# Kernel optimization log

Hardware: AMD Instinct MI355X
Metric: run time of the kernel (lower is better)

The kernel has to match this reference:

```python
import jax, jax.numpy as jnp
import numpy as np

BATCH = 262144
LATENT_DIM = 128
N_CLUSTERS = 10


def setup_inputs() -> dict:
    key = jax.random.key(0)
    kz, kc = jax.random.split(key)
    z = jax.random.normal(kz, (BATCH, LATENT_DIM), dtype=jnp.float32)
    cluster_centers = jax.random.normal(kc, (N_CLUSTERS, LATENT_DIM), dtype=jnp.float32)
    return {"z": z, "cluster_centers": cluster_centers}


def reference(z, cluster_centers):
    # Student's-t soft assignment (alpha = 1):
    # q_ij = (1 + ||z_i - mu_j||^2)^-1, power ((alpha+1)/2) == 1
    # squared distances: [B, K]
    sq_dist = jnp.sum(jnp.square(z[:, None, :] - cluster_centers[None, :, :]), axis=2)
    q = 1.0 / (1.0 + sq_dist)
    q = q ** ((1.0 + 1.0) / 2.0)
    q = q / jnp.sum(q, axis=1, keepdims=True)  # row-normalize

    # target distribution p
    weight = q ** 2 / jnp.sum(q, axis=0)            # [B, K] / [K]
    p = weight / jnp.sum(weight, axis=1, keepdims=True)
    return (q, p)
```

## Files before the change

kernel.cpp:

```cpp
#include <hip/hip_runtime.h>
#include <stdint.h>

#define NB 262144
#define D 128
#define K 10

#define QBLOCKS 1024
#define QTHREADS 256
#define ROWS_PER_BLOCK (NB / QBLOCKS)
#define TILES_PER_WAVE (ROWS_PER_BLOCK / 4 / 16)

typedef __attribute__((ext_vector_type(8))) __bf16 bf16x8;
typedef __attribute__((ext_vector_type(4))) float f32x4;

__device__ inline __bf16 f2bf(float x) {
  unsigned u = __builtin_bit_cast(unsigned, x);
  u += 0x7fffu + ((u >> 16) & 1u);
  unsigned short s = (unsigned short)(u >> 16);
  return __builtin_bit_cast(__bf16, s);
}

__device__ inline bf16x8 make_frag(float4 lo, float4 hi) {
  bf16x8 a;
  a[0] = f2bf(lo.x); a[1] = f2bf(lo.y); a[2] = f2bf(lo.z); a[3] = f2bf(lo.w);
  a[4] = f2bf(hi.x); a[5] = f2bf(hi.y); a[6] = f2bf(hi.z); a[7] = f2bf(hi.w);
  return a;
}

__global__ __launch_bounds__(QTHREADS) void qkern(
    const float* __restrict__ z, const float* __restrict__ centers,
    float* __restrict__ qout, float* __restrict__ f) {
  __shared__ float red[4][16];

  const int t = threadIdx.x;
  const int w = t >> 6;
  const int lane = t & 63;
  const int n = lane & 15;
  const int g = lane >> 4;

  bf16x8 bfrag[4];
  float mu2 = 0.f;
  if (n < K) {
    const float* cp = centers + n * D;
#pragma unroll
    for (int c = 0; c < 4; ++c) {
      float4 lo = *reinterpret_cast<const float4*>(cp + c * 32 + g * 8);
      float4 hi = *reinterpret_cast<const float4*>(cp + c * 32 + g * 8 + 4);
      bfrag[c] = make_frag(lo, hi);
    }
#pragma unroll
    for (int d4 = 0; d4 < 32; ++d4) {
      float4 v = *reinterpret_cast<const float4*>(cp + d4 * 4);
      mu2 = fmaf(v.x, v.x, mu2); mu2 = fmaf(v.y, v.y, mu2);
      mu2 = fmaf(v.z, v.z, mu2); mu2 = fmaf(v.w, v.w, mu2);
    }
  } else {
    unsigned short zb = 0;
#pragma unroll
    for (int c = 0; c < 4; ++c)
#pragma unroll
      for (int j = 0; j < 8; ++j) bfrag[c][j] = __builtin_bit_cast(__bf16, zb);
  }

  float colp = 0.f;
  const int wbase = blockIdx.x * ROWS_PER_BLOCK + w * (TILES_PER_WAVE * 16);

  for (int tile = 0; tile < TILES_PER_WAVE; ++tile) {
    const int rbase = wbase + tile * 16;
    const float* zr = z + (size_t)(rbase + n) * D + g * 8;

    float4 zf[8];
#pragma unroll
    for (int c = 0; c < 4; ++c) {
      zf[2 * c]     = *reinterpret_cast<const float4*>(zr + c * 32);
      zf[2 * c + 1] = *reinterpret_cast<const float4*>(zr + c * 32 + 4);
    }

    float z2 = 0.f;
#pragma unroll
    for (int q8 = 0; q8 < 8; ++q8) {
      z2 = fmaf(zf[q8].x, zf[q8].x, z2); z2 = fmaf(zf[q8].y, zf[q8].y, z2);
      z2 = fmaf(zf[q8].z, zf[q8].z, z2); z2 = fmaf(zf[q8].w, zf[q8].w, z2);
    }
    z2 += __shfl_xor(z2, 16);
    z2 += __shfl_xor(z2, 32);

    f32x4 acc = {0.f, 0.f, 0.f, 0.f};
#pragma unroll
    for (int c = 0; c < 4; ++c) {
      bf16x8 a = make_frag(zf[2 * c], zf[2 * c + 1]);
      acc = __builtin_amdgcn_mfma_f32_16x16x32_bf16(a, bfrag[c], acc, 0, 0, 0);
    }

#pragma unroll
    for (int i = 0; i < 4; ++i) {
      float z2i = __shfl(z2, g * 4 + i);
      float d2 = z2i - 2.f * acc[i] + mu2;
      float qu = (n < K) ? 1.0f / (1.0f + d2) : 0.f;
      float rs = qu;
      rs += __shfl_xor(rs, 1); rs += __shfl_xor(rs, 2);
      rs += __shfl_xor(rs, 4); rs += __shfl_xor(rs, 8);
      float qv = qu * (1.0f / rs);
      if (n < K) qout[(size_t)(rbase + g * 4 + i) * K + n] = qv;
      colp += qv;
    }
  }

  colp += __shfl_xor(colp, 16);
  colp += __shfl_xor(colp, 32);
  if (lane < 16) red[w][lane] = colp;
  __syncthreads();
  if (t < K) atomicAdd(&f[t], red[0][t] + red[1][t] + red[2][t] + red[3][t]);
}

__global__ __launch_bounds__(256) void pkern(
    const float* __restrict__ q, const float* __restrict__ f,
    float* __restrict__ p) {
  int row = blockIdx.x * 256 + threadIdx.x;
  const float* qr = q + (size_t)row * K;
  float wv[K];
  float s = 0.f;
#pragma unroll
  for (int j = 0; j < K; j += 2) {
    float2 qq = *reinterpret_cast<const float2*>(&qr[j]);
    wv[j] = qq.x * qq.x / f[j];
    wv[j + 1] = qq.y * qq.y / f[j + 1];
    s += wv[j] + wv[j + 1];
  }
  float inv = 1.0f / s;
  float* pr = p + (size_t)row * K;
#pragma unroll
  for (int j = 0; j < K; j += 2) {
    *reinterpret_cast<float2*>(&pr[j]) = make_float2(wv[j] * inv, wv[j + 1] * inv);
  }
}

extern "C" void kernel_launch(void* const* d_in, const int* in_sizes, int n_in,
                              void* d_out, int out_size, void* d_ws, size_t ws_size,
                              hipStream_t stream) {
  const float* z = (const float*)d_in[0];
  const float* centers = (const float*)d_in[1];
  float* out = (float*)d_out;
  float* f = (float*)d_ws;

  hipMemsetAsync(d_ws, 0, K * sizeof(float), stream);
  qkern<<<QBLOCKS, QTHREADS, 0, stream>>>(z, centers, out, f);
  pkern<<<NB / 256, 256, 0, stream>>>(out, f, out + (size_t)NB * K);
}
```

Before: 210.1 us.

## Transpose MFMA operands so rows map to lanes, vectorize q stores, shrink blocks

Swaps the MFMA operand roles so centers are the A operand and z rows the B operand, which puts each row's cluster values in a single lane group. Row normalization then takes two cross-lane shuffles, and q can be written with float4/float2 stores instead of scattered scalar stores. The block now covers 128 rows with a fully unrolled two-tile loop, giving many more blocks and more per-block atomics on the column sums. It also replaces the manual bf16 rounding with native casts.

```diff
diff --git a/kernel.cpp b/kernel.cpp
--- a/kernel.cpp
+++ b/kernel.cpp
@@ -5,25 +5,17 @@
 #define D 128
 #define K 10
 
-#define QBLOCKS 1024
+#define ROWS_PER_BLOCK 128
+#define QBLOCKS (NB / ROWS_PER_BLOCK)
 #define QTHREADS 256
-#define ROWS_PER_BLOCK (NB / QBLOCKS)
-#define TILES_PER_WAVE (ROWS_PER_BLOCK / 4 / 16)
 
 typedef __attribute__((ext_vector_type(8))) __bf16 bf16x8;
 typedef __attribute__((ext_vector_type(4))) float f32x4;
 
-__device__ inline __bf16 f2bf(float x) {
-  unsigned u = __builtin_bit_cast(unsigned, x);
-  u += 0x7fffu + ((u >> 16) & 1u);
-  unsigned short s = (unsigned short)(u >> 16);
-  return __builtin_bit_cast(__bf16, s);
-}
-
-__device__ inline bf16x8 make_frag(float4 lo, float4 hi) {
+__device__ inline bf16x8 make_frag(const float4 lo, const float4 hi) {
   bf16x8 a;
-  a[0] = f2bf(lo.x); a[1] = f2bf(lo.y); a[2] = f2bf(lo.z); a[3] = f2bf(lo.w);
-  a[4] = f2bf(hi.x); a[5] = f2bf(hi.y); a[6] = f2bf(hi.z); a[7] = f2bf(hi.w);
+  a[0] = (__bf16)lo.x; a[1] = (__bf16)lo.y; a[2] = (__bf16)lo.z; a[3] = (__bf16)lo.w;
+  a[4] = (__bf16)hi.x; a[5] = (__bf16)hi.y; a[6] = (__bf16)hi.z; a[7] = (__bf16)hi.w;
   return a;
 }
 
@@ -38,34 +30,38 @@
   const int n = lane & 15;
   const int g = lane >> 4;
 
-  bf16x8 bfrag[4];
-  float mu2 = 0.f;
+  bf16x8 afrag[4];
+  float mu2own = 0.f;
   if (n < K) {
     const float* cp = centers + n * D;
 #pragma unroll
     for (int c = 0; c < 4; ++c) {
       float4 lo = *reinterpret_cast<const float4*>(cp + c * 32 + g * 8);
       float4 hi = *reinterpret_cast<const float4*>(cp + c * 32 + g * 8 + 4);
-      bfrag[c] = make_frag(lo, hi);
+      afrag[c] = make_frag(lo, hi);
     }
 #pragma unroll
     for (int d4 = 0; d4 < 32; ++d4) {
       float4 v = *reinterpret_cast<const float4*>(cp + d4 * 4);
-      mu2 = fmaf(v.x, v.x, mu2); mu2 = fmaf(v.y, v.y, mu2);
-      mu2 = fmaf(v.z, v.z, mu2); mu2 = fmaf(v.w, v.w, mu2);
+      mu2own = fmaf(v.x, v.x, mu2own); mu2own = fmaf(v.y, v.y, mu2own);
+      mu2own = fmaf(v.z, v.z, mu2own); mu2own = fmaf(v.w, v.w, mu2own);
     }
   } else {
     unsigned short zb = 0;
 #pragma unroll
     for (int c = 0; c < 4; ++c)
 #pragma unroll
-      for (int j = 0; j < 8; ++j) bfrag[c][j] = __builtin_bit_cast(__bf16, zb);
+      for (int j = 0; j < 8; ++j) afrag[c][j] = __builtin_bit_cast(__bf16, zb);
   }
+  float mu2[4];
+#pragma unroll
+  for (int i = 0; i < 4; ++i) mu2[i] = __shfl(mu2own, g * 4 + i);
 
-  float colp = 0.f;
-  const int wbase = blockIdx.x * ROWS_PER_BLOCK + w * (TILES_PER_WAVE * 16);
+  float colp[4] = {0.f, 0.f, 0.f, 0.f};
+  const int wbase = blockIdx.x * ROWS_PER_BLOCK + w * 32;
 
-  for (int tile = 0; tile < TILES_PER_WAVE; ++tile) {
+#pragma unroll
+  for (int tile = 0; tile < 2; ++tile) {
     const int rbase = wbase + tile * 16;
     const float* zr = z + (size_t)(rbase + n) * D + g * 8;
 
@@ -88,27 +84,43 @@
     f32x4 acc = {0.f, 0.f, 0.f, 0.f};
 #pragma unroll
     for (int c = 0; c < 4; ++c) {
-      bf16x8 a = make_frag(zf[2 * c], zf[2 * c + 1]);
-      acc = __builtin_amdgcn_mfma_f32_16x16x32_bf16(a, bfrag[c], acc, 0, 0, 0);
+      bf16x8 b = make_frag(zf[2 * c], zf[2 * c + 1]);
+      acc = __builtin_amdgcn_mfma_f32_16x16x32_bf16(afrag[c], b, acc, 0, 0, 0);
     }
 
+    float qu[4];
+    float s = 0.f;
 #pragma unroll
     for (int i = 0; i < 4; ++i) {
-      float z2i = __shfl(z2, g * 4 + i);
-      float d2 = z2i - 2.f * acc[i] + mu2;
-      float qu = (n < K) ? 1.0f / (1.0f + d2) : 0.f;
-      float rs = qu;
-      rs += __shfl_xor(rs, 1); rs += __shfl_xor(rs, 2);
-      rs += __shfl_xor(rs, 4); rs += __shfl_xor(rs, 8);
-      float qv = qu * (1.0f / rs);
-      if (n < K) qout[(size_t)(rbase + g * 4 + i) * K + n] = qv;
-      colp += qv;
+      const int cl = g * 4 + i;
+      float d2 = z2 - 2.f * acc[i] + mu2[i];
+      qu[i] = (cl < K) ? 1.0f / (1.0f + d2) : 0.f;
+      s += qu[i];
     }
+    s += __shfl_xor(s, 16);
+    s += __shfl_xor(s, 32);
+    float inv = 1.0f / s;
+#pragma unroll
+    for (int i = 0; i < 4; ++i) { qu[i] *= inv; colp[i] += qu[i]; }
+
+    float* qo = qout + (size_t)(rbase + n) * K;
+    if (g < 2)
+      *reinterpret_cast<float4*>(qo + g * 4) = make_float4(qu[0], qu[1], qu[2], qu[3]);
+    else if (g == 2)
+      *reinterpret_cast<float2*>(qo + 8) = make_float2(qu[0], qu[1]);
   }
 
-  colp += __shfl_xor(colp, 16);
-  colp += __shfl_xor(colp, 32);
-  if (lane < 16) red[w][lane] = colp;
+#pragma unroll
+  for (int i = 0; i < 4; ++i) {
+    colp[i] += __shfl_xor(colp[i], 1);
+    colp[i] += __shfl_xor(colp[i], 2);
+    colp[i] += __shfl_xor(colp[i], 4);
+    colp[i] += __shfl_xor(colp[i], 8);
+  }
+  if (n == 0) {
+#pragma unroll
+    for (int i = 0; i < 4; ++i) red[w][g * 4 + i] = colp[i];
+  }
   __syncthreads();
   if (t < K) atomicAdd(&f[t], red[0][t] + red[1][t] + red[2][t] + red[3][t]);
 }
```

Result: no change. 206.8 us (-1.6%).
